# Kernel tuning notes

Hardware: AMD Instinct MI355X
Metric: run time of the kernel (lower is better)

Reference implementation:

```python
import jax, jax.numpy as jnp
import numpy as np

B, S = 32, 10  # hard-coded in original call()/reshape


def setup_inputs() -> dict:
    key = jax.random.key(0)
    k1, k2, k3 = jax.random.split(key, 3)
    D, K = 4096, 8192
    p = jax.random.normal(k1, (B, S, D), dtype=jnp.float32)
    q = jax.random.normal(k2, (B, S, D), dtype=jnp.float32)
    W = jax.random.uniform(k3, (K, D), dtype=jnp.float32)  # 'uniform' initializer
    return {"p": p, "q": q, "W": W}


def reference(p, q, W):
    # Multi-perspective matching: for each perspective k, weight p rows and the
    # last q state by W[k], then cosine distance = -mean(l2norm(a)*l2norm(b)).
    # Vectorized over (batch, perspective, seq) via einsums on W^2 -- never
    # materializes the (B,K,S,D) weighted tensors.
    D = p.shape[-1]
    W2 = W * W                                   # (K, D)
    q_last = q[:, -1, :]                          # (B, D)
    # dot(w*q_last, w*p_s) = sum_d p*q_last*W^2
    dot = jnp.einsum('bsd,kd->bks', p * q_last[:, None, :], W2)   # (B, K, S)
    norm_p = jnp.sqrt(jnp.einsum('bsd,kd->bks', p * p, W2))       # (B, K, S)
    norm_q = jnp.sqrt(jnp.einsum('bd,kd->bk', q_last * q_last, W2))  # (B, K)
    dist = -dot / (norm_p * norm_q[:, :, None] * D)  # -mean of normalized product
    # original concatenates over k then s per batch, then reshapes to (32,10,K)
    return dist.reshape(B, S, -1)
```

## Files before the change

### kernel.cpp

```cpp
#include <hip/hip_runtime.h>
#include <stdint.h>

#define B_ 32
#define S_ 10
#define D_ 4096
#define K_ 8192
#define RPB 21
#define M_REAL (B_ * RPB)

#define BM 256
#define BN 128
#define BK 32
#define M_PAD_MF 768
#define KSPLIT 4
#define KCHUNK (D_ / KSPLIT)
#define NSTEP (KCHUNK / BK)

typedef _Float16 f16x8 __attribute__((ext_vector_type(8)));
typedef float f32x4 __attribute__((ext_vector_type(4)));
typedef unsigned short us4 __attribute__((ext_vector_type(4)));

__device__ __forceinline__ void async16(const void* g, void* l) {
  __builtin_amdgcn_global_load_lds(
      (const __attribute__((address_space(1))) unsigned int*)g,
      (__attribute__((address_space(3))) unsigned int*)l, 16, 0, 0);
}

__global__ __launch_bounds__(256)
void build_a_f16(const float* __restrict__ p, const float* __restrict__ q,
                 unsigned short* __restrict__ Af) {
  size_t idx = (size_t)blockIdx.x * 256 + threadIdx.x;
  int d4 = (int)(idx & 1023);
  int m = (int)(idx >> 10);
  float4 v = make_float4(0.f, 0.f, 0.f, 0.f);
  if (m < M_REAL) {
    int b = m / RPB;
    int r = m - b * RPB;
    const float4* q4 = (const float4*)(q + (size_t)(b * S_ + (S_ - 1)) * D_);
    if (r < S_) {
      const float4* p4 = (const float4*)(p + (size_t)(b * S_ + r) * D_);
      float4 pv = p4[d4]; float4 qv = q4[d4];
      v = make_float4(pv.x * qv.x, pv.y * qv.y, pv.z * qv.z, pv.w * qv.w);
    } else if (r < 2 * S_) {
      const float4* p4 = (const float4*)(p + (size_t)(b * S_ + (r - S_)) * D_);
      float4 pv = p4[d4];
      v = make_float4(pv.x * pv.x, pv.y * pv.y, pv.z * pv.z, pv.w * pv.w);
    } else {
      float4 qv = q4[d4];
      v = make_float4(qv.x * qv.x, qv.y * qv.y, qv.z * qv.z, qv.w * qv.w);
    }
  }
  us4 h;
  ((unsigned short*)&h)[0] = (unsigned short)__builtin_bit_cast(unsigned short, (_Float16)v.x);
  ((unsigned short*)&h)[1] = (unsigned short)__builtin_bit_cast(unsigned short, (_Float16)v.y);
  ((unsigned short*)&h)[2] = (unsigned short)__builtin_bit_cast(unsigned short, (_Float16)v.z);
  ((unsigned short*)&h)[3] = (unsigned short)__builtin_bit_cast(unsigned short, (_Float16)v.w);
  ((us4*)Af)[idx] = h;
}

__global__ __launch_bounds__(512, 4)
void gemm_mfma(const unsigned short* __restrict__ Af, const float* __restrict__ W,
               float* __restrict__ G) {
  __shared__ unsigned short lds[32768];
  const int tid = threadIdx.x;
  const int lane = tid & 63;
  const int wid = tid >> 6;
  const int m0 = blockIdx.y * BM;
  const int n0 = blockIdx.x * BN;
  const int ks = blockIdx.z;
  const int d_base = ks * KCHUNK;

  char* const ldsb = (char*)lds;
  char* const ldsWf = ldsb + 32768;

  const unsigned short* gpA[2];
  uint32_t ldsoffA[2];
#pragma unroll
  for (int e = 0; e < 2; ++e) {
    int c = e * 512 + tid;
    int row = c >> 2;
    int g = (tid & 3) ^ ((row ^ (row >> 2)) & 3);
    gpA[e] = Af + (size_t)(m0 + row) * D_ + d_base + g * 8;
    ldsoffA[e] = (uint32_t)(e * 8192 + wid * 1024);
  }

  const float* gpW[2];
  uint32_t ldsoffW[2];
#pragma unroll
  for (int e = 0; e < 2; ++e) {
    int c = e * 512 + tid;
    int row = c >> 3;
    int g = (tid & 7) ^ (row & 7);
    gpW[e] = W + (size_t)(n0 + row) * D_ + d_base + g * 4;
    ldsoffW[e] = (uint32_t)(e * 8192 + wid * 1024);
  }

  f32x4 acc[4][4];
#pragma unroll
  for (int i = 0; i < 4; ++i)
#pragma unroll
    for (int j = 0; j < 4; ++j) acc[i][j] = (f32x4){0.f, 0.f, 0.f, 0.f};

  const int wm = wid >> 1;
  const int wn = wid & 1;
  const int frow = lane & 15;
  const int k16 = lane >> 4;
  int aoff[4];
  int woffL[4], woffH[4];
#pragma unroll
  for (int f = 0; f < 4; ++f) {
    int ra = wm * 64 + f * 16 + frow;
    aoff[f] = ra * 64 + ((k16 ^ ((ra ^ (ra >> 2)) & 3)) * 16);
    int rw = wn * 64 + f * 16 + frow;
    woffL[f] = rw * 128 + (((2 * k16) ^ (rw & 7)) * 16);
    woffH[f] = rw * 128 + (((2 * k16 + 1) ^ (rw & 7)) * 16);
  }

  async16(gpA[0], ldsb + ldsoffA[0]);
  async16(gpA[1], ldsb + ldsoffA[1]);
  async16(gpW[0], ldsWf + ldsoffW[0]);
  async16(gpW[1], ldsWf + ldsoffW[1]);
  __syncthreads();

  for (int i = 0; i < NSTEP; ++i) {
    const int dn = ((i + 1 < NSTEP) ? (i + 1) : i) * BK;
    const uint32_t nb = (uint32_t)(((i + 1) & 1) * 16384);
    async16(gpA[0] + dn, ldsb + nb + ldsoffA[0]);
    async16(gpA[1] + dn, ldsb + nb + ldsoffA[1]);
    async16(gpW[0] + dn, ldsWf + nb + ldsoffW[0]);
    async16(gpW[1] + dn, ldsWf + nb + ldsoffW[1]);

    const uint32_t cb = (uint32_t)((i & 1) * 16384);
    f16x8 aF[4];
#pragma unroll
    for (int f = 0; f < 4; ++f)
      aF[f] = *(const f16x8*)(ldsb + cb + aoff[f]);
#pragma unroll
    for (int nf = 0; nf < 4; ++nf) {
      f32x4 lo = *(const f32x4*)(ldsWf + cb + woffL[nf]);
      f32x4 hi = *(const f32x4*)(ldsWf + cb + woffH[nf]);
      f16x8 wF;
      wF[0] = (_Float16)(lo[0] * lo[0]); wF[1] = (_Float16)(lo[1] * lo[1]);
      wF[2] = (_Float16)(lo[2] * lo[2]); wF[3] = (_Float16)(lo[3] * lo[3]);
      wF[4] = (_Float16)(hi[0] * hi[0]); wF[5] = (_Float16)(hi[1] * hi[1]);
      wF[6] = (_Float16)(hi[2] * hi[2]); wF[7] = (_Float16)(hi[3] * hi[3]);
#pragma unroll
      for (int mf = 0; mf < 4; ++mf)
        acc[mf][nf] = __builtin_amdgcn_mfma_f32_16x16x32_f16(aF[mf], wF, acc[mf][nf], 0, 0, 0);
    }

    __syncthreads();
  }

  float* Gp = G + (size_t)ks * M_PAD_MF * K_;
  const int crow = m0 + wm * 64;
  const int ccol = n0 + wn * 64;
#pragma unroll
  for (int mf = 0; mf < 4; ++mf)
#pragma unroll
    for (int nf = 0; nf < 4; ++nf)
#pragma unroll
      for (int r = 0; r < 4; ++r) {
        int row = crow + mf * 16 + (lane >> 4) * 4 + r;
        int col = ccol + nf * 16 + (lane & 15);
        Gp[(size_t)row * K_ + col] = acc[mf][nf][r];
      }
}

__global__ __launch_bounds__(256)
void epilogue4(const float* __restrict__ G, float* __restrict__ out) {
  __shared__ float buf[256 * S_];
  const int tid = threadIdx.x;
  const int b = blockIdx.y;
  const int k0 = blockIdx.x * 256;
  const int k = k0 + tid;
  const size_t PL = (size_t)M_PAD_MF * K_;
  const float* Gb = G + (size_t)b * RPB * K_ + k;
  float nq = sqrtf(Gb[20 * K_] + Gb[PL + 20 * K_] + Gb[2 * PL + 20 * K_] + Gb[3 * PL + 20 * K_]);
#pragma unroll
  for (int s = 0; s < S_; ++s) {
    size_t od = (size_t)s * K_;
    size_t op = (size_t)(S_ + s) * K_;
    float dot = Gb[od] + Gb[PL + od] + Gb[2 * PL + od] + Gb[3 * PL + od];
    float pp  = Gb[op] + Gb[PL + op] + Gb[2 * PL + op] + Gb[3 * PL + op];
    buf[tid * S_ + s] = -dot / (sqrtf(pp) * nq * (float)D_);
  }
  __syncthreads();
  float* ob = out + ((size_t)b * K_ + k0) * S_;
  for (int i = tid; i < 256 * S_; i += 256) ob[i] = buf[i];
}

extern "C" void kernel_launch(void* const* d_in, const int* in_sizes, int n_in,
                              void* d_out, int out_size, void* d_ws, size_t ws_size,
                              hipStream_t stream) {
  const float* p = (const float*)d_in[0];
  const float* q = (const float*)d_in[1];
  const float* W = (const float*)d_in[2];
  float* out = (float*)d_out;

  uint8_t* w = (uint8_t*)d_ws;
  unsigned short* Af = (unsigned short*)w;
  float* G = (float*)(w + 6291456);

  build_a_f16<<<(M_PAD_MF * (D_ / 4)) / 256, 256, 0, stream>>>(p, q, Af);
  dim3 ggrid(K_ / BN, M_PAD_MF / BM, KSPLIT);
  gemm_mfma<<<ggrid, 512, 0, stream>>>(Af, W, G);
  epilogue4<<<dim3(K_ / 256, B_), 256, 0, stream>>>(G, out);
}
```

Measured before the change: 121.0 us.

## Enlarge GEMM tile to 256x256, raise split-K to 8, skip padded rows

```diff
diff --git a/kernel.cpp b/kernel.cpp
--- a/kernel.cpp
+++ b/kernel.cpp
@@ -9,10 +9,10 @@
 #define M_REAL (B_ * RPB)
 
 #define BM 256
-#define BN 128
+#define BN 256
 #define BK 32
 #define M_PAD_MF 768
-#define KSPLIT 4
+#define KSPLIT 8
 #define KCHUNK (D_ / KSPLIT)
 #define NSTEP (KCHUNK / BK)
 
@@ -58,10 +58,10 @@
   ((us4*)Af)[idx] = h;
 }
 
-__global__ __launch_bounds__(512, 4)
+__global__ __launch_bounds__(512, 2)
 void gemm_mfma(const unsigned short* __restrict__ Af, const float* __restrict__ W,
                float* __restrict__ G) {
-  __shared__ unsigned short lds[32768];
+  __shared__ unsigned short lds[49152];
   const int tid = threadIdx.x;
   const int lane = tid & 63;
   const int wid = tid >> 6;
@@ -70,119 +70,131 @@
   const int ks = blockIdx.z;
   const int d_base = ks * KCHUNK;
 
-  char* const ldsb = (char*)lds;
-  char* const ldsWf = ldsb + 32768;
+  char* const ldsA = (char*)lds;
+  char* const ldsW = (char*)lds + 32768;
 
   const unsigned short* gpA[2];
-  uint32_t ldsoffA[2];
+  uint32_t offA[2];
 #pragma unroll
   for (int e = 0; e < 2; ++e) {
     int c = e * 512 + tid;
     int row = c >> 2;
-    int g = (tid & 3) ^ ((row ^ (row >> 2)) & 3);
+    int g = (c & 3) ^ ((row ^ (row >> 2)) & 3);
     gpA[e] = Af + (size_t)(m0 + row) * D_ + d_base + g * 8;
-    ldsoffA[e] = (uint32_t)(e * 8192 + wid * 1024);
-  }
-
-  const float* gpW[2];
-  uint32_t ldsoffW[2];
-#pragma unroll
-  for (int e = 0; e < 2; ++e) {
+    offA[e] = (uint32_t)(c * 16);
+  }
+
+  const float* gpW[4];
+  uint32_t offW[4];
+#pragma unroll
+  for (int e = 0; e < 4; ++e) {
     int c = e * 512 + tid;
     int row = c >> 3;
-    int g = (tid & 7) ^ (row & 7);
+    int g = (c & 7) ^ (row & 7);
     gpW[e] = W + (size_t)(n0 + row) * D_ + d_base + g * 4;
-    ldsoffW[e] = (uint32_t)(e * 8192 + wid * 1024);
-  }
-
-  f32x4 acc[4][4];
-#pragma unroll
-  for (int i = 0; i < 4; ++i)
+    offW[e] = (uint32_t)(c * 16);
+  }
+
+  f32x4 acc[8][4];
+#pragma unroll
+  for (int i = 0; i < 8; ++i)
 #pragma unroll
     for (int j = 0; j < 4; ++j) acc[i][j] = (f32x4){0.f, 0.f, 0.f, 0.f};
 
-  const int wm = wid >> 1;
-  const int wn = wid & 1;
+  const int wm = wid >> 2;
+  const int wn = wid & 3;
   const int frow = lane & 15;
   const int k16 = lane >> 4;
-  int aoff[4];
+  int aoff[8];
   int woffL[4], woffH[4];
 #pragma unroll
+  for (int f = 0; f < 8; ++f) {
+    int ra = wm * 128 + f * 16 + frow;
+    aoff[f] = ra * 64 + ((k16 ^ ((ra ^ (ra >> 2)) & 3)) * 16);
+  }
+#pragma unroll
   for (int f = 0; f < 4; ++f) {
-    int ra = wm * 64 + f * 16 + frow;
-    aoff[f] = ra * 64 + ((k16 ^ ((ra ^ (ra >> 2)) & 3)) * 16);
     int rw = wn * 64 + f * 16 + frow;
     woffL[f] = rw * 128 + (((2 * k16) ^ (rw & 7)) * 16);
     woffH[f] = rw * 128 + (((2 * k16 + 1) ^ (rw & 7)) * 16);
   }
 
-  async16(gpA[0], ldsb + ldsoffA[0]);
-  async16(gpA[1], ldsb + ldsoffA[1]);
-  async16(gpW[0], ldsWf + ldsoffW[0]);
-  async16(gpW[1], ldsWf + ldsoffW[1]);
+#pragma unroll
+  for (int e = 0; e < 2; ++e) async16(gpA[e], ldsA + offA[e]);
+#pragma unroll
+  for (int e = 0; e < 4; ++e) async16(gpW[e], ldsW + offW[e]);
   __syncthreads();
 
   for (int i = 0; i < NSTEP; ++i) {
     const int dn = ((i + 1 < NSTEP) ? (i + 1) : i) * BK;
-    const uint32_t nb = (uint32_t)(((i + 1) & 1) * 16384);
-    async16(gpA[0] + dn, ldsb + nb + ldsoffA[0]);
-    async16(gpA[1] + dn, ldsb + nb + ldsoffA[1]);
-    async16(gpW[0] + dn, ldsWf + nb + ldsoffW[0]);
-    async16(gpW[1] + dn, ldsWf + nb + ldsoffW[1]);
-
-    const uint32_t cb = (uint32_t)((i & 1) * 16384);
-    f16x8 aF[4];
-#pragma unroll
-    for (int f = 0; f < 4; ++f)
-      aF[f] = *(const f16x8*)(ldsb + cb + aoff[f]);
+    const uint32_t nbA = (uint32_t)(((i + 1) & 1) * 16384);
+    const uint32_t nbW = (uint32_t)(((i + 1) & 1) * 32768);
+#pragma unroll
+    for (int e = 0; e < 2; ++e) async16(gpA[e] + dn, ldsA + nbA + offA[e]);
+#pragma unroll
+    for (int e = 0; e < 4; ++e) async16(gpW[e] + dn, ldsW + nbW + offW[e]);
+
+    char* const cA = ldsA + (uint32_t)((i & 1) * 16384);
+    char* const cW = ldsW + (uint32_t)((i & 1) * 32768);
+    f16x8 aF[8];
+#pragma unroll
+    for (int f = 0; f < 8; ++f)
+      aF[f] = *(const f16x8*)(cA + aoff[f]);
 #pragma unroll
     for (int nf = 0; nf < 4; ++nf) {
-      f32x4 lo = *(const f32x4*)(ldsWf + cb + woffL[nf]);
-      f32x4 hi = *(const f32x4*)(ldsWf + cb + woffH[nf]);
+      f32x4 lo = *(const f32x4*)(cW + woffL[nf]);
+      f32x4 hi = *(const f32x4*)(cW + woffH[nf]);
       f16x8 wF;
       wF[0] = (_Float16)(lo[0] * lo[0]); wF[1] = (_Float16)(lo[1] * lo[1]);
       wF[2] = (_Float16)(lo[2] * lo[2]); wF[3] = (_Float16)(lo[3] * lo[3]);
       wF[4] = (_Float16)(hi[0] * hi[0]); wF[5] = (_Float16)(hi[1] * hi[1]);
       wF[6] = (_Float16)(hi[2] * hi[2]); wF[7] = (_Float16)(hi[3] * hi[3]);
 #pragma unroll
-      for (int mf = 0; mf < 4; ++mf)
+      for (int mf = 0; mf < 8; ++mf)
         acc[mf][nf] = __builtin_amdgcn_mfma_f32_16x16x32_f16(aF[mf], wF, acc[mf][nf], 0, 0, 0);
     }
 
     __syncthreads();
   }
 
-  float* Gp = G + (size_t)ks * M_PAD_MF * K_;
-  const int crow = m0 + wm * 64;
+  float* Gp = G + (size_t)ks * M_REAL * K_;
+  const int crow = m0 + wm * 128;
   const int ccol = n0 + wn * 64;
 #pragma unroll
-  for (int mf = 0; mf < 4; ++mf)
+  for (int mf = 0; mf < 8; ++mf)
 #pragma unroll
     for (int nf = 0; nf < 4; ++nf)
 #pragma unroll
       for (int r = 0; r < 4; ++r) {
         int row = crow + mf * 16 + (lane >> 4) * 4 + r;
         int col = ccol + nf * 16 + (lane & 15);
-        Gp[(size_t)row * K_ + col] = acc[mf][nf][r];
+        if (row < M_REAL) Gp[(size_t)row * K_ + col] = acc[mf][nf][r];
       }
 }
 
 __global__ __launch_bounds__(256)
-void epilogue4(const float* __restrict__ G, float* __restrict__ out) {
+void epilogue8(const float* __restrict__ G, float* __restrict__ out) {
   __shared__ float buf[256 * S_];
   const int tid = threadIdx.x;
   const int b = blockIdx.y;
   const int k0 = blockIdx.x * 256;
   const int k = k0 + tid;
-  const size_t PL = (size_t)M_PAD_MF * K_;
+  const size_t PL = (size_t)M_REAL * K_;
   const float* Gb = G + (size_t)b * RPB * K_ + k;
-  float nq = sqrtf(Gb[20 * K_] + Gb[PL + 20 * K_] + Gb[2 * PL + 20 * K_] + Gb[3 * PL + 20 * K_]);
+  float nqs = 0.f;
+#pragma unroll
+  for (int pl = 0; pl < KSPLIT; ++pl) nqs += Gb[pl * PL + 20 * K_];
+  float nq = sqrtf(nqs);
 #pragma unroll
   for (int s = 0; s < S_; ++s) {
     size_t od = (size_t)s * K_;
     size_t op = (size_t)(S_ + s) * K_;
-    float dot = Gb[od] + Gb[PL + od] + Gb[2 * PL + od] + Gb[3 * PL + od];
-    float pp  = Gb[op] + Gb[PL + op] + Gb[2 * PL + op] + Gb[3 * PL + op];
+    float dot = 0.f, pp = 0.f;
+#pragma unroll
+    for (int pl = 0; pl < KSPLIT; ++pl) {
+      dot += Gb[pl * PL + od];
+      pp  += Gb[pl * PL + op];
+    }
     buf[tid * S_ + s] = -dot / (sqrtf(pp) * nq * (float)D_);
   }
   __syncthreads();
@@ -205,5 +217,5 @@
   build_a_f16<<<(M_PAD_MF * (D_ / 4)) / 256, 256, 0, stream>>>(p, q, Af);
   dim3 ggrid(K_ / BN, M_PAD_MF / BM, KSPLIT);
   gemm_mfma<<<ggrid, 512, 0, stream>>>(Af, W, G);
-  epilogue4<<<dim3(K_ / 256, B_), 256, 0, stream>>>(G, out);
-}
+  epilogue8<<<dim3(K_ / 256, B_), 256, 0, stream>>>(G, out);
+}
```

Measured after the change: 153.2 us. 26.7% more time.
